# Kernel optimization log

Hardware: AMD Instinct MI355X
Metric: run time of the kernel (lower is better)

Reference implementation:

```python
import jax, jax.numpy as jnp
import numpy as np

N = 100000
E = 1600000
D_IN = 128
F = 128


def _glorot(key, shape, scale=1.0):
    fan_in, fan_out = shape
    std = jnp.sqrt(2.0 / (fan_in + fan_out))
    return jax.random.normal(key, shape, dtype=jnp.float32) * std * scale


def setup_inputs() -> dict:
    key = jax.random.key(0)
    ks = jax.random.split(key, 10)
    h = jax.random.normal(ks[0], (N, D_IN), dtype=jnp.float32)
    # ensure every node appears as a row (src) so degree >= 1 (no inf in deg**-0.5)
    src_extra = jax.random.randint(ks[1], (E - N,), 0, N, dtype=jnp.int32)
    edge_src = jnp.concatenate([jnp.arange(N, dtype=jnp.int32), src_extra])
    edge_dst = jax.random.randint(ks[2], (E,), 0, N, dtype=jnp.int32)
    # faithful to original: fake indices sampled in [0, E) (jnp indexing clamps)
    src_fake = jax.random.randint(ks[3], (E,), 0, E, dtype=jnp.int32)
    dst_fake = jax.random.randint(ks[4], (E,), 0, E, dtype=jnp.int32)
    w_gcn0 = _glorot(ks[5], (D_IN, F))
    w_gcn1 = _glorot(ks[6], (F, F))
    # small scale on rate0 head to keep exp(sum over F dims) finite in fp32
    w_rate0 = _glorot(ks[7], (F, F), scale=0.05)
    w_rate1 = _glorot(ks[8], (F, 1))
    w_alpha = _glorot(ks[9], (F, 1))
    return {"h": h, "w_gcn0": w_gcn0, "w_gcn1": w_gcn1, "w_rate0": w_rate0,
            "w_rate1": w_rate1, "w_alpha": w_alpha, "edge_src": edge_src,
            "edge_dst": edge_dst, "src_fake": src_fake, "dst_fake": dst_fake}


def _gcn(h, W, norm, edge_src, edge_dst):
    h = h * norm                     # [N, d] degree pre-norm
    h = h @ W                        # dense projection
    h = jax.ops.segment_sum(h[edge_dst], edge_src, num_segments=N)  # a @ h
    return h * norm                  # degree post-norm


def reference(h, w_gcn0, w_gcn1, w_rate0, w_rate1, w_alpha,
              edge_src, edge_dst, src_fake, dst_fake):
    ones = jnp.ones((E,), dtype=h.dtype)
    deg = jax.ops.segment_sum(ones, edge_src, num_segments=N)  # row sums of a
    norm = (deg ** -0.5)[:, None]

    h = _gcn(h, w_gcn0, norm, edge_src, edge_dst)
    h = _gcn(h, w_gcn1, norm, edge_src, edge_dst)

    rate0 = h @ w_rate0   # [N, F]
    rate1 = h @ w_rate1   # [N, 1]
    alpha = h @ w_alpha   # [N, 1]

    src, dst = edge_src, edge_dst
    rate0_real = jnp.exp((rate0[src] + rate0[dst]).sum(-1))
    rate1_real = jnp.exp((rate1[src] + rate1[dst]).sum(-1))
    alpha_real = jax.nn.sigmoid((alpha[src] * alpha[dst]).sum(-1) / alpha.shape[-1] ** 0.5)

    # faithful to original (including rate0+rate1 mix and /shape (not sqrt) in alpha_fake)
    rate0_fake = jnp.exp((rate0[src_fake] + rate1[dst_fake]).sum(-1))
    rate1_fake = jnp.exp((rate1[src_fake] + rate1[dst_fake]).sum(-1))
    alpha_fake = jax.nn.sigmoid((alpha[src] * alpha[dst_fake]).sum(-1) / alpha.shape[-1])

    return jnp.stack([rate0_real, rate1_real, alpha_real,
                      rate0_fake, rate1_fake, alpha_fake])  # [6, E]
```

## Files before the change

kernel.cpp:

```cpp
#include <hip/hip_runtime.h>
#include <hip/hip_bf16.h>
#include <math.h>

#define NN 100000
#define EE 1600000
#define KB 256
#define RR 391
#define CAP 8192


__global__ __launch_bounds__(256) void k_initcur(int* __restrict__ gcur) {
    gcur[threadIdx.x] = threadIdx.x * CAP;
}


__global__ __launch_bounds__(256) void k_partA(const int* __restrict__ src, const int* __restrict__ dst,
                                               int* __restrict__ gcur, unsigned int* __restrict__ pk, int E) {
    __shared__ int cnt[KB];
    __shared__ int base[KB];
    int t = threadIdx.x;
    int e0 = blockIdx.x * 4096;
    cnt[t] = 0;
    __syncthreads();
    unsigned int pkv[16];
    int bkt[16];
    #pragma unroll
    for (int i = 0; i < 16; ++i) {
        int e = e0 + i * 256 + t;
        if (e < E) {
            int s = src[e];
            int d = dst[e];
            int b = s / RR;
            bkt[i] = b;
            pkv[i] = (unsigned int)d | ((unsigned int)(s - b * RR) << 17);
            atomicAdd(&cnt[b], 1);
        } else {
            bkt[i] = -1;
        }
    }
    __syncthreads();
    base[t] = (cnt[t] > 0) ? atomicAdd(&gcur[t], cnt[t]) : 0;
    __syncthreads();
    cnt[t] = 0;
    __syncthreads();
    #pragma unroll
    for (int i = 0; i < 16; ++i) {
        if (bkt[i] >= 0) {
            int r = atomicAdd(&cnt[bkt[i]], 1);
            int pos = base[bkt[i]] + r;
            if (pos < (bkt[i] + 1) * CAP) pk[pos] = pkv[i];
        }
    }
}


__global__ __launch_bounds__(128) void k_pmat(const float* __restrict__ w_gcn0,
                                              const float* __restrict__ w_gcn1,
                                              const float* __restrict__ w_rate0,
                                              const float* __restrict__ w_rate1,
                                              const float* __restrict__ w_alpha,
                                              float* __restrict__ Pt0, float* __restrict__ Pt1,
                                              float* __restrict__ Pt2) {
    __shared__ float V0[128], V1[128], V2[128];
    __shared__ float Q0[128], Q1[128], Q2[128];
    int t = threadIdx.x;
    float s = 0.f;
    for (int j = 0; j < 128; ++j) s += w_rate0[t * 128 + j];
    V0[t] = s;
    V1[t] = w_rate1[t];
    V2[t] = w_alpha[t];
    __syncthreads();
    {
        float q0 = 0.f, q1 = 0.f, q2 = 0.f;
        for (int k = 0; k < 128; ++k) {
            float w = w_gcn1[t * 128 + k];
            q0 += w * V0[k];
            q1 += w * V1[k];
            q2 += w * V2[k];
        }
        Q0[t] = q0; Q1[t] = q1; Q2[t] = q2;
    }
    __syncthreads();
    {
        float p0 = 0.f, p1 = 0.f, p2 = 0.f;
        for (int m = 0; m < 128; ++m) {
            float w = w_gcn0[t * 128 + m];
            p0 += w * Q0[m];
            p1 += w * Q1[m];
            p2 += w * Q2[m];
        }
        Pt0[t] = p0; Pt1[t] = p1; Pt2[t] = p2;
    }
}


__global__ __launch_bounds__(1024) void k_cnt_proj(const unsigned int* __restrict__ pk,
                                                   const int* __restrict__ gcur,
                                                   const float* __restrict__ h,
                                                   const float* __restrict__ Pt0, const float* __restrict__ Pt1,
                                                   const float* __restrict__ Pt2,
                                                   float* __restrict__ nrm, float4* __restrict__ w4, int n) {
    __shared__ int c[RR];
    __shared__ float s_nrm[RR];
    __shared__ float sP0[128], sP1[128], sP2[128];
    int b = blockIdx.x;
    int t = threadIdx.x;
    int nlo = b * RR;
    int nhi = nlo + RR; if (nhi > n) nhi = n;
    if (nlo >= n) return;
    int nn = nhi - nlo;
    if (t < 128) { sP0[t] = Pt0[t]; sP1[t] = Pt1[t]; sP2[t] = Pt2[t]; }
    for (int i = t; i < RR; i += 1024) c[i] = 0;
    __syncthreads();
    int P0 = b * CAP;
    int m = gcur[b] - P0;
    for (int i = t; i < m; i += 1024) atomicAdd(&c[pk[P0 + i] >> 17], 1);
    __syncthreads();
    for (int i = t; i < nn; i += 1024) {
        float nv = rsqrtf((float)c[i]);
        s_nrm[i] = nv;
        nrm[nlo + i] = nv;
    }
    __syncthreads();
    int hw = t >> 5;
    int l32 = t & 31;
    int c4 = l32 * 4;
    float4 c0 = *(const float4*)(sP0 + c4);
    float4 c1 = *(const float4*)(sP1 + c4);
    float4 c2 = *(const float4*)(sP2 + c4);
    for (int i0 = 0; i0 < nn; i0 += 32) {
        int i = i0 + hw;
        if (i >= nn) break;
        int node = nlo + i;
        float4 hv = *(const float4*)(h + (size_t)node * 128 + c4);
        float p0 = hv.x * c0.x + hv.y * c0.y + hv.z * c0.z + hv.w * c0.w;
        float p1 = hv.x * c1.x + hv.y * c1.y + hv.z * c1.z + hv.w * c1.w;
        float p2 = hv.x * c2.x + hv.y * c2.y + hv.z * c2.z + hv.w * c2.w;
        #pragma unroll
        for (int off = 16; off > 0; off >>= 1) {
            p0 += __shfl_down(p0, off, 32);
            p1 += __shfl_down(p1, off, 32);
            p2 += __shfl_down(p2, off, 32);
        }
        if (l32 == 0) {
            float nv = s_nrm[i];
            w4[node] = make_float4(nv * p0, nv * p1, nv * p2, 0.f);
        }
    }
}


__global__ __launch_bounds__(1024) void k_agg(const unsigned int* __restrict__ pk,
                                              const int* __restrict__ gcur,
                                              const float4* __restrict__ T, const float* __restrict__ nrm,
                                              float4* __restrict__ outv, int n, int mode) {
    __shared__ float s0[RR], s1[RR], s2[RR];
    int b = blockIdx.x;
    int t = threadIdx.x;
    int nlo = b * RR;
    int nhi = nlo + RR; if (nhi > n) nhi = n;
    if (nlo >= n) return;
    for (int i = t; i < RR; i += 1024) { s0[i] = 0.f; s1[i] = 0.f; s2[i] = 0.f; }
    __syncthreads();
    int P0 = b * CAP;
    int m = gcur[b] - P0;
    for (int i = t; i < m; i += 1024) {
        unsigned int w = pk[P0 + i];
        int srel = (int)(w >> 17);
        float4 v = T[w & 0x1FFFFu];
        atomicAdd(&s0[srel], v.x);
        atomicAdd(&s1[srel], v.y);
        atomicAdd(&s2[srel], v.z);
    }
    __syncthreads();
    int nn = nhi - nlo;
    for (int i = t; i < nn; i += 1024) {
        int node = nlo + i;
        float nv = nrm[node];
        float sc = (mode == 1) ? nv * nv : nv;
        outv[node] = make_float4(sc * s0[i], sc * s1[i], sc * s2[i], 0.f);
    }
}


__global__ __launch_bounds__(256) void k_edge_out(const int* __restrict__ esrc, const int* __restrict__ edst,
                                                  const int* __restrict__ sfake, const int* __restrict__ dfake,
                                                  const float4* __restrict__ p4, float* __restrict__ out,
                                                  int E, int n) {
    int e = blockIdx.x * 256 + threadIdx.x;
    if (e >= E) return;
    int s = esrc[e], d = edst[e];
    int sf = sfake[e]; sf = sf < 0 ? 0 : (sf >= n ? n - 1 : sf);
    int df = dfake[e]; df = df < 0 ? 0 : (df >= n ? n - 1 : df);
    float4 ps = p4[s], pd = p4[d], psf = p4[sf], pdf = p4[df];
    out[e]                 = expf(ps.x + pd.x);
    out[(size_t)E + e]     = expf(ps.y + pd.y);
    out[(size_t)2 * E + e] = 1.f / (1.f + expf(-(ps.z * pd.z)));
    out[(size_t)3 * E + e] = expf(psf.x + 128.f * pdf.y);
    out[(size_t)4 * E + e] = expf(psf.y + pdf.y);
    out[(size_t)5 * E + e] = 1.f / (1.f + expf(-(ps.z * pdf.z)));
}


extern "C" void kernel_launch(void* const* d_in, const int* in_sizes, int n_in,
                              void* d_out, int out_size, void* d_ws, size_t ws_size,
                              hipStream_t stream) {
    const float* h       = (const float*)d_in[0];
    const float* w_gcn0  = (const float*)d_in[1];
    const float* w_gcn1  = (const float*)d_in[2];
    const float* w_rate0 = (const float*)d_in[3];
    const float* w_rate1 = (const float*)d_in[4];
    const float* w_alpha = (const float*)d_in[5];
    const int* edge_src  = (const int*)d_in[6];
    const int* edge_dst  = (const int*)d_in[7];
    const int* src_fake  = (const int*)d_in[8];
    const int* dst_fake  = (const int*)d_in[9];
    float* out = (float*)d_out;

    const int N = NN, E = EE;

    char* p = (char*)d_ws;
    auto alloc = [&](size_t bytes) {
        char* r = p;
        p += (bytes + 255) & ~(size_t)255;
        return r;
    };
    unsigned int* pk = (unsigned int*)alloc((size_t)KB * CAP * 4);
    int* gcur   = (int*)alloc(KB * 4);
    float* nrm  = (float*)alloc((size_t)N * 4);
    float4* w4  = (float4*)alloc((size_t)N * 16);
    float4* z4  = (float4*)alloc((size_t)N * 16);
    float4* p4  = (float4*)alloc((size_t)N * 16);
    float* Pt0  = (float*)alloc(512);
    float* Pt1  = (float*)alloc(512);
    float* Pt2  = (float*)alloc(512);

    int ebl4k = (E + 4095) / 4096;
    int ebl = (E + 255) / 256;

    k_initcur<<<1, KB, 0, stream>>>(gcur);
    k_partA<<<ebl4k, 256, 0, stream>>>(edge_src, edge_dst, gcur, pk, E);
    k_pmat<<<1, 128, 0, stream>>>(w_gcn0, w_gcn1, w_rate0, w_rate1, w_alpha, Pt0, Pt1, Pt2);
    k_cnt_proj<<<KB, 1024, 0, stream>>>(pk, gcur, h, Pt0, Pt1, Pt2, nrm, w4, N);
    k_agg<<<KB, 1024, 0, stream>>>(pk, gcur, w4, nrm, z4, N, 1);
    k_agg<<<KB, 1024, 0, stream>>>(pk, gcur, z4, nrm, p4, N, 2);
    k_edge_out<<<ebl, 256, 0, stream>>>(edge_src, edge_dst, src_fake, dst_fake, p4, out, E, N);
}
```

Before: 238.6 us.

## Fuse all stages into one cooperative persistent kernel with grid syncs

```diff
diff --git a/kernel.cpp b/kernel.cpp
--- a/kernel.cpp
+++ b/kernel.cpp
@@ -1,204 +1,204 @@
 #include <hip/hip_runtime.h>
-#include <hip/hip_bf16.h>
+#include <hip/hip_cooperative_groups.h>
 #include <math.h>
+
+namespace cg = cooperative_groups;
 
 #define NN 100000
 #define EE 1600000
 #define KB 256
 #define RR 391
 #define CAP 8192
-
-
-__global__ __launch_bounds__(256) void k_initcur(int* __restrict__ gcur) {
-    gcur[threadIdx.x] = threadIdx.x * CAP;
-}
-
-
-__global__ __launch_bounds__(256) void k_partA(const int* __restrict__ src, const int* __restrict__ dst,
-                                               int* __restrict__ gcur, unsigned int* __restrict__ pk, int E) {
-    __shared__ int cnt[KB];
-    __shared__ int base[KB];
-    int t = threadIdx.x;
-    int e0 = blockIdx.x * 4096;
-    cnt[t] = 0;
-    __syncthreads();
-    unsigned int pkv[16];
-    int bkt[16];
-    #pragma unroll
-    for (int i = 0; i < 16; ++i) {
-        int e = e0 + i * 256 + t;
-        if (e < E) {
-            int s = src[e];
-            int d = dst[e];
-            int b = s / RR;
-            bkt[i] = b;
-            pkv[i] = (unsigned int)d | ((unsigned int)(s - b * RR) << 17);
-            atomicAdd(&cnt[b], 1);
-        } else {
-            bkt[i] = -1;
-        }
-    }
-    __syncthreads();
-    base[t] = (cnt[t] > 0) ? atomicAdd(&gcur[t], cnt[t]) : 0;
-    __syncthreads();
-    cnt[t] = 0;
-    __syncthreads();
-    #pragma unroll
-    for (int i = 0; i < 16; ++i) {
-        if (bkt[i] >= 0) {
-            int r = atomicAdd(&cnt[bkt[i]], 1);
-            int pos = base[bkt[i]] + r;
-            if (pos < (bkt[i] + 1) * CAP) pk[pos] = pkv[i];
-        }
-    }
-}
-
-
-__global__ __launch_bounds__(128) void k_pmat(const float* __restrict__ w_gcn0,
-                                              const float* __restrict__ w_gcn1,
-                                              const float* __restrict__ w_rate0,
-                                              const float* __restrict__ w_rate1,
-                                              const float* __restrict__ w_alpha,
-                                              float* __restrict__ Pt0, float* __restrict__ Pt1,
-                                              float* __restrict__ Pt2) {
-    __shared__ float V0[128], V1[128], V2[128];
-    __shared__ float Q0[128], Q1[128], Q2[128];
-    int t = threadIdx.x;
-    float s = 0.f;
-    for (int j = 0; j < 128; ++j) s += w_rate0[t * 128 + j];
-    V0[t] = s;
-    V1[t] = w_rate1[t];
-    V2[t] = w_alpha[t];
-    __syncthreads();
-    {
+#define EPB 6250
+#define EITER 7
+
+
+__global__ __launch_bounds__(1024) void k_fused(
+    const float* __restrict__ h,
+    const float* __restrict__ w_gcn0,
+    const float* __restrict__ w_gcn1,
+    const float* __restrict__ w_rate0,
+    const float* __restrict__ w_rate1,
+    const float* __restrict__ w_alpha,
+    const int* __restrict__ esrc,
+    const int* __restrict__ edst,
+    const int* __restrict__ sfake,
+    const int* __restrict__ dfake,
+    unsigned int* __restrict__ pk,
+    int* __restrict__ gcur,
+    float4* __restrict__ w4,
+    float4* __restrict__ z4,
+    float4* __restrict__ p4,
+    float* __restrict__ out)
+{
+    __shared__ unsigned int s_pk[CAP];
+    __shared__ int   s_s[EPB];
+    __shared__ int   s_d[EPB];
+    __shared__ alignas(16) float sP0[128];
+    __shared__ alignas(16) float sP1[128];
+    __shared__ alignas(16) float sP2[128];
+    __shared__ int   c[RR];
+    __shared__ float s_nrm[RR];
+    __shared__ float s0[RR], s1[RR], s2[RR];
+    __shared__ int   cnt[KB], base[KB];
+
+    cg::grid_group grid = cg::this_grid();
+    const int b = blockIdx.x;
+    const int t = threadIdx.x;
+
+    if (t < KB) cnt[t] = 0;
+    if (t < 128) {
+        float s = 0.f;
+        for (int j = 0; j < 128; ++j) s += w_rate0[t * 128 + j];
+        s0[t] = s;
+        s1[t] = w_rate1[t];
+        s2[t] = w_alpha[t];
+    }
+    __syncthreads();
+    if (t < 128) {
         float q0 = 0.f, q1 = 0.f, q2 = 0.f;
         for (int k = 0; k < 128; ++k) {
             float w = w_gcn1[t * 128 + k];
-            q0 += w * V0[k];
-            q1 += w * V1[k];
-            q2 += w * V2[k];
-        }
-        Q0[t] = q0; Q1[t] = q1; Q2[t] = q2;
-    }
-    __syncthreads();
-    {
+            q0 += w * s0[k]; q1 += w * s1[k]; q2 += w * s2[k];
+        }
+        s0[128 + t] = q0; s1[128 + t] = q1; s2[128 + t] = q2;
+    }
+    __syncthreads();
+    if (t < 128) {
         float p0 = 0.f, p1 = 0.f, p2 = 0.f;
         for (int m = 0; m < 128; ++m) {
             float w = w_gcn0[t * 128 + m];
-            p0 += w * Q0[m];
-            p1 += w * Q1[m];
-            p2 += w * Q2[m];
-        }
-        Pt0[t] = p0; Pt1[t] = p1; Pt2[t] = p2;
-    }
-}
-
-
-__global__ __launch_bounds__(1024) void k_cnt_proj(const unsigned int* __restrict__ pk,
-                                                   const int* __restrict__ gcur,
-                                                   const float* __restrict__ h,
-                                                   const float* __restrict__ Pt0, const float* __restrict__ Pt1,
-                                                   const float* __restrict__ Pt2,
-                                                   float* __restrict__ nrm, float4* __restrict__ w4, int n) {
-    __shared__ int c[RR];
-    __shared__ float s_nrm[RR];
-    __shared__ float sP0[128], sP1[128], sP2[128];
-    int b = blockIdx.x;
-    int t = threadIdx.x;
-    int nlo = b * RR;
-    int nhi = nlo + RR; if (nhi > n) nhi = n;
-    if (nlo >= n) return;
-    int nn = nhi - nlo;
-    if (t < 128) { sP0[t] = Pt0[t]; sP1[t] = Pt1[t]; sP2[t] = Pt2[t]; }
-    for (int i = t; i < RR; i += 1024) c[i] = 0;
-    __syncthreads();
-    int P0 = b * CAP;
-    int m = gcur[b] - P0;
-    for (int i = t; i < m; i += 1024) atomicAdd(&c[pk[P0 + i] >> 17], 1);
-    __syncthreads();
-    for (int i = t; i < nn; i += 1024) {
-        float nv = rsqrtf((float)c[i]);
-        s_nrm[i] = nv;
-        nrm[nlo + i] = nv;
-    }
-    __syncthreads();
-    int hw = t >> 5;
-    int l32 = t & 31;
-    int c4 = l32 * 4;
-    float4 c0 = *(const float4*)(sP0 + c4);
-    float4 c1 = *(const float4*)(sP1 + c4);
-    float4 c2 = *(const float4*)(sP2 + c4);
-    for (int i0 = 0; i0 < nn; i0 += 32) {
-        int i = i0 + hw;
-        if (i >= nn) break;
-        int node = nlo + i;
-        float4 hv = *(const float4*)(h + (size_t)node * 128 + c4);
-        float p0 = hv.x * c0.x + hv.y * c0.y + hv.z * c0.z + hv.w * c0.w;
-        float p1 = hv.x * c1.x + hv.y * c1.y + hv.z * c1.z + hv.w * c1.w;
-        float p2 = hv.x * c2.x + hv.y * c2.y + hv.z * c2.z + hv.w * c2.w;
-        #pragma unroll
-        for (int off = 16; off > 0; off >>= 1) {
-            p0 += __shfl_down(p0, off, 32);
-            p1 += __shfl_down(p1, off, 32);
-            p2 += __shfl_down(p2, off, 32);
-        }
-        if (l32 == 0) {
-            float nv = s_nrm[i];
-            w4[node] = make_float4(nv * p0, nv * p1, nv * p2, 0.f);
-        }
-    }
-}
-
-
-__global__ __launch_bounds__(1024) void k_agg(const unsigned int* __restrict__ pk,
-                                              const int* __restrict__ gcur,
-                                              const float4* __restrict__ T, const float* __restrict__ nrm,
-                                              float4* __restrict__ outv, int n, int mode) {
-    __shared__ float s0[RR], s1[RR], s2[RR];
-    int b = blockIdx.x;
-    int t = threadIdx.x;
-    int nlo = b * RR;
-    int nhi = nlo + RR; if (nhi > n) nhi = n;
-    if (nlo >= n) return;
-    for (int i = t; i < RR; i += 1024) { s0[i] = 0.f; s1[i] = 0.f; s2[i] = 0.f; }
-    __syncthreads();
-    int P0 = b * CAP;
-    int m = gcur[b] - P0;
+            p0 += w * s0[128 + m]; p1 += w * s1[128 + m]; p2 += w * s2[128 + m];
+        }
+        sP0[t] = p0; sP1[t] = p1; sP2[t] = p2;
+    }
+    __syncthreads();
+
+    const int e0 = b * EPB;
+    unsigned int pkv[EITER];
+    int bkt[EITER];
+    #pragma unroll
+    for (int r = 0; r < EITER; ++r) {
+        int i = r * 1024 + t;
+        if (i < EPB) {
+            int s = esrc[e0 + i];
+            int d = edst[e0 + i];
+            s_s[i] = s; s_d[i] = d;
+            int bb = s / RR;
+            bkt[r] = bb;
+            pkv[r] = (unsigned int)d | ((unsigned int)(s - bb * RR) << 17);
+            atomicAdd(&cnt[bb], 1);
+        } else bkt[r] = -1;
+    }
+    __syncthreads();
+    if (t < KB) base[t] = cnt[t] ? atomicAdd(&gcur[t], cnt[t]) : 0;
+    __syncthreads();
+    if (t < KB) cnt[t] = 0;
+    __syncthreads();
+    #pragma unroll
+    for (int r = 0; r < EITER; ++r) {
+        if (bkt[r] >= 0) {
+            int rr = atomicAdd(&cnt[bkt[r]], 1);
+            int rel = base[bkt[r]] + rr;
+            if (rel < CAP) pk[bkt[r] * CAP + rel] = pkv[r];
+        }
+    }
+    grid.sync();
+
+    const int P0 = b * CAP;
+    int m = gcur[b]; if (m > CAP) m = CAP;
+    const int nlo = b * RR;
+    const int nn  = (NN - nlo) < RR ? (NN - nlo) : RR;
+    if (t < RR) c[t] = 0;
+    __syncthreads();
     for (int i = t; i < m; i += 1024) {
         unsigned int w = pk[P0 + i];
+        s_pk[i] = w;
+        atomicAdd(&c[w >> 17], 1);
+    }
+    __syncthreads();
+    if (t < nn) s_nrm[t] = rsqrtf((float)c[t]);
+    __syncthreads();
+    {
+        const int hw  = t >> 5;
+        const int l32 = t & 31;
+        const int c4  = l32 * 4;
+        float4 c0 = *(const float4*)(sP0 + c4);
+        float4 c1 = *(const float4*)(sP1 + c4);
+        float4 c2 = *(const float4*)(sP2 + c4);
+        for (int i0 = 0; i0 < nn; i0 += 32) {
+            int i = i0 + hw;
+            if (i >= nn) break;
+            int node = nlo + i;
+            float4 hv = *(const float4*)(h + (size_t)node * 128 + c4);
+            float p0v = hv.x * c0.x + hv.y * c0.y + hv.z * c0.z + hv.w * c0.w;
+            float p1v = hv.x * c1.x + hv.y * c1.y + hv.z * c1.z + hv.w * c1.w;
+            float p2v = hv.x * c2.x + hv.y * c2.y + hv.z * c2.z + hv.w * c2.w;
+            #pragma unroll
+            for (int off = 16; off > 0; off >>= 1) {
+                p0v += __shfl_down(p0v, off, 32);
+                p1v += __shfl_down(p1v, off, 32);
+                p2v += __shfl_down(p2v, off, 32);
+            }
+            if (l32 == 0) {
+                float nv = s_nrm[i];
+                w4[node] = make_float4(nv * p0v, nv * p1v, nv * p2v, 0.f);
+            }
+        }
+    }
+    grid.sync();
+
+    if (t < RR) { s0[t] = 0.f; s1[t] = 0.f; s2[t] = 0.f; }
+    __syncthreads();
+    for (int i = t; i < m; i += 1024) {
+        unsigned int w = s_pk[i];
+        float4 v = w4[w & 0x1FFFFu];
         int srel = (int)(w >> 17);
-        float4 v = T[w & 0x1FFFFu];
         atomicAdd(&s0[srel], v.x);
         atomicAdd(&s1[srel], v.y);
         atomicAdd(&s2[srel], v.z);
     }
     __syncthreads();
-    int nn = nhi - nlo;
-    for (int i = t; i < nn; i += 1024) {
-        int node = nlo + i;
-        float nv = nrm[node];
-        float sc = (mode == 1) ? nv * nv : nv;
-        outv[node] = make_float4(sc * s0[i], sc * s1[i], sc * s2[i], 0.f);
-    }
-}
-
-
-__global__ __launch_bounds__(256) void k_edge_out(const int* __restrict__ esrc, const int* __restrict__ edst,
-                                                  const int* __restrict__ sfake, const int* __restrict__ dfake,
-                                                  const float4* __restrict__ p4, float* __restrict__ out,
-                                                  int E, int n) {
-    int e = blockIdx.x * 256 + threadIdx.x;
-    if (e >= E) return;
-    int s = esrc[e], d = edst[e];
-    int sf = sfake[e]; sf = sf < 0 ? 0 : (sf >= n ? n - 1 : sf);
-    int df = dfake[e]; df = df < 0 ? 0 : (df >= n ? n - 1 : df);
-    float4 ps = p4[s], pd = p4[d], psf = p4[sf], pdf = p4[df];
-    out[e]                 = expf(ps.x + pd.x);
-    out[(size_t)E + e]     = expf(ps.y + pd.y);
-    out[(size_t)2 * E + e] = 1.f / (1.f + expf(-(ps.z * pd.z)));
-    out[(size_t)3 * E + e] = expf(psf.x + 128.f * pdf.y);
-    out[(size_t)4 * E + e] = expf(psf.y + pdf.y);
-    out[(size_t)5 * E + e] = 1.f / (1.f + expf(-(ps.z * pdf.z)));
+    if (t < nn) {
+        float nv = s_nrm[t], sc = nv * nv;
+        z4[nlo + t] = make_float4(sc * s0[t], sc * s1[t], sc * s2[t], 0.f);
+    }
+    grid.sync();
+
+    if (t < RR) { s0[t] = 0.f; s1[t] = 0.f; s2[t] = 0.f; }
+    __syncthreads();
+    for (int i = t; i < m; i += 1024) {
+        unsigned int w = s_pk[i];
+        float4 v = z4[w & 0x1FFFFu];
+        int srel = (int)(w >> 17);
+        atomicAdd(&s0[srel], v.x);
+        atomicAdd(&s1[srel], v.y);
+        atomicAdd(&s2[srel], v.z);
+    }
+    __syncthreads();
+    if (t < nn) {
+        float nv = s_nrm[t];
+        p4[nlo + t] = make_float4(nv * s0[t], nv * s1[t], nv * s2[t], 0.f);
+    }
+    grid.sync();
+
+    #pragma unroll
+    for (int r = 0; r < EITER; ++r) {
+        int i = r * 1024 + t;
+        if (i < EPB) {
+            int e = e0 + i;
+            int s = s_s[i], d = s_d[i];
+            int sf = sfake[e]; sf = sf < 0 ? 0 : (sf >= NN ? NN - 1 : sf);
+            int df = dfake[e]; df = df < 0 ? 0 : (df >= NN ? NN - 1 : df);
+            float4 ps = p4[s], pd = p4[d], psf = p4[sf], pdf = p4[df];
+            out[e]                  = expf(ps.x + pd.x);
+            out[(size_t)EE + e]     = expf(ps.y + pd.y);
+            out[(size_t)2 * EE + e] = 1.f / (1.f + expf(-(ps.z * pd.z)));
+            out[(size_t)3 * EE + e] = expf(psf.x + 128.f * pdf.y);
+            out[(size_t)4 * EE + e] = expf(psf.y + pdf.y);
+            out[(size_t)5 * EE + e] = 1.f / (1.f + expf(-(ps.z * pdf.z)));
+        }
+    }
 }
 
 
@@ -217,8 +217,6 @@
     const int* dst_fake  = (const int*)d_in[9];
     float* out = (float*)d_out;
 
-    const int N = NN, E = EE;
-
     char* p = (char*)d_ws;
     auto alloc = [&](size_t bytes) {
         char* r = p;
@@ -227,22 +225,14 @@
     };
     unsigned int* pk = (unsigned int*)alloc((size_t)KB * CAP * 4);
     int* gcur   = (int*)alloc(KB * 4);
-    float* nrm  = (float*)alloc((size_t)N * 4);
-    float4* w4  = (float4*)alloc((size_t)N * 16);
-    float4* z4  = (float4*)alloc((size_t)N * 16);
-    float4* p4  = (float4*)alloc((size_t)N * 16);
-    float* Pt0  = (float*)alloc(512);
-    float* Pt1  = (float*)alloc(512);
-    float* Pt2  = (float*)alloc(512);
-
-    int ebl4k = (E + 4095) / 4096;
-    int ebl = (E + 255) / 256;
-
-    k_initcur<<<1, KB, 0, stream>>>(gcur);
-    k_partA<<<ebl4k, 256, 0, stream>>>(edge_src, edge_dst, gcur, pk, E);
-    k_pmat<<<1, 128, 0, stream>>>(w_gcn0, w_gcn1, w_rate0, w_rate1, w_alpha, Pt0, Pt1, Pt2);
-    k_cnt_proj<<<KB, 1024, 0, stream>>>(pk, gcur, h, Pt0, Pt1, Pt2, nrm, w4, N);
-    k_agg<<<KB, 1024, 0, stream>>>(pk, gcur, w4, nrm, z4, N, 1);
-    k_agg<<<KB, 1024, 0, stream>>>(pk, gcur, z4, nrm, p4, N, 2);
-    k_edge_out<<<ebl, 256, 0, stream>>>(edge_src, edge_dst, src_fake, dst_fake, p4, out, E, N);
+    float4* w4  = (float4*)alloc((size_t)NN * 16);
+    float4* z4  = (float4*)alloc((size_t)NN * 16);
+    float4* p4  = (float4*)alloc((size_t)NN * 16);
+
+    hipMemsetAsync(gcur, 0, KB * sizeof(int), stream);
+
+    void* args[] = { &h, &w_gcn0, &w_gcn1, &w_rate0, &w_rate1, &w_alpha,
+                     &edge_src, &edge_dst, &src_fake, &dst_fake,
+                     &pk, &gcur, &w4, &z4, &p4, &out };
+    hipLaunchCooperativeKernel((void*)k_fused, dim3(KB), dim3(1024), args, 0, stream);
 }
```

After: 392.5 us. 1.65x slower.
